# Performance work log

Hardware: AMD Instinct MI355X
Metric: run time of the kernel (lower is better)

## Reference

```python
import jax, jax.numpy as jnp
import numpy as np

WS = 8      # window size (all three entries equal)
NH = 4      # num_heads
CE = 32     # exp_channels = layer_size[0]


def _sine_pos(h, w, npf, temperature=10000.0):
    # faithful port of get_sine_position_encoding(HW=(h,w), num_pos_feats=npf, normalize=True)
    scale = 2.0 * np.pi
    eps = 1e-6
    y = np.cumsum(np.ones((1, h, w), np.float32), 1)
    xg = np.cumsum(np.ones((1, h, w), np.float32), 2)
    y = y / (y[:, -1:, :] + eps) * scale
    xg = xg / (xg[:, :, -1:] + eps) * scale
    dim_t = temperature ** (2.0 * (np.arange(npf) // 2) / npf)
    px = xg[..., None] / dim_t
    py = y[..., None] / dim_t
    px = np.stack((np.sin(px[..., 0::2]), np.cos(px[..., 1::2])), -1).reshape(1, h, w, npf)
    py = np.stack((np.sin(py[..., 0::2]), np.cos(py[..., 1::2])), -1).reshape(1, h, w, npf)
    return jnp.asarray(np.concatenate((py, px), -1).reshape(1, h * w, 2 * npf), jnp.float32)


def _rel_pos_index(a, b):
    coords = np.stack(np.meshgrid(np.arange(a), np.arange(b), indexing='ij')).reshape(2, -1)
    rel = (coords[:, :, None] - coords[:, None, :]).transpose(1, 2, 0).copy()
    rel[..., 0] += a - 1
    rel[..., 1] += b - 1
    rel[..., 0] *= 2 * b - 1
    return jnp.asarray(rel.sum(-1).astype(np.int32))


POS_BIAS = _sine_pos(WS, WS, CE // 2)   # (1, 64, 32)
RPI = _rel_pos_index(WS, WS)            # (64, 64) int


def _ln(x, g, b, eps=1e-5):
    mu = x.mean(-1, keepdims=True)
    var = jnp.mean((x - mu) ** 2, -1, keepdims=True)
    return (x - mu) / jnp.sqrt(var + eps) * g + b


def _geglu(x, w11, b11, w12, b12, w2, b2):
    return (jax.nn.gelu(x @ w11.T + b11, approximate=False) * (x @ w12.T + b12)) @ w2.T + b2


def _forward(x, ln1_g, ln1_b, w_ea, w_sa, rpb_table, fc11_w, fc11_b, fc12_w, fc12_b, fc2_w, fc2_b, ln2_g, ln2_b, m11_w, m11_b, m12_w, m12_b, m2_w, m2_b):
    B, E, C, H, W = x.shape
    h, w = H // WS, W // WS
    N = WS * WS
    nW = h * w
    scale = C ** (-0.5)
    x_origin = x
    # window partition (matches torch view/permute/contiguous-view exactly)
    xw = x.reshape(B, E, C, h, WS, w, WS).transpose(0, 1, 3, 5, 2, 4, 6).reshape(-1, N, C)
    xw = _ln(xw, ln1_g, ln1_b)
    # fused QKV projections
    qkv_ea = ((xw + POS_BIAS) @ w_ea.T).reshape(B, 4, nW, N, 3, NH, C)
    qkv_ea = qkv_ea.transpose(1, 4, 0, 2, 5, 3, 6).reshape(4, 3, B * nW, NH, N, C)   # E nP (B nW) nH W C
    qkv_sa = (xw @ w_sa.T).reshape(B, 4, nW, N, 3, NH, C)
    qkv_sa = qkv_sa.transpose(4, 0, 2, 5, 3, 1, 6).reshape(3, B * nW, NH, N, 4 * C)  # nP (B nW) nH W (E C)

    def attn(q, k, v, bias=None):
        s = jnp.einsum('bhid,bhjd->bhij', q * scale, k)
        if bias is not None:
            s = s + bias
        return jnp.einsum('bhij,bhjd->bhid', jax.nn.softmax(s, axis=-1), v)

    # exposure-alignment branches (the Python loop over 4 exposures, vectorized)
    ea1 = jax.vmap(attn, in_axes=(None, 0, 0))(qkv_ea[0, 0], qkv_ea[:, 1], qkv_ea[:, 2])
    ea2 = jax.vmap(attn, in_axes=(0, None, None))(qkv_ea[:, 0], qkv_ea[0, 1], qkv_ea[0, 2])

    def merge(o):  # (4, BnW, NH, N, C) -> cat over exposures on channels -> (BnW, N, NH*4C)
        o = jnp.moveaxis(o, 0, 3).reshape(B * nW, NH, N, 4 * C)
        return o.transpose(0, 2, 1, 3).reshape(B * nW, N, NH * 4 * C)

    ea1, ea2 = merge(ea1), merge(ea2)
    # self-attention branch with relative position bias gather
    bias = rpb_table[RPI.reshape(-1)].reshape(N, N, NH).transpose(2, 0, 1)[None]
    sa = attn(qkv_sa[0], qkv_sa[1], qkv_sa[2], bias)
    sa = sa.transpose(0, 2, 1, 3).reshape(B * nW, N, NH * 4 * C)

    y = jnp.concatenate([sa, ea1, ea2], axis=-1)                      # (BnW, N, 12*NH*C)
    y = _geglu(y, fc11_w, fc11_b, fc12_w, fc12_b, fc2_w, fc2_b)       # (BnW, N, 4C)
    # window reverse (matches torch view/permute/view exactly)
    y = y.reshape(B, h, w, WS, WS, 4, NH, C // NH).transpose(0, 5, 6, 7, 3, 1, 4, 2).reshape(B, 4, C, H, W)
    x1 = y + x_origin
    t = x1.transpose(0, 3, 4, 1, 2).reshape(B, H, W, 4 * C)           # B N C H W -> B H W (N C)
    t = _ln(t, ln2_g, ln2_b)
    t = _geglu(t, m11_w, m11_b, m12_w, m12_b, m2_w, m2_b)
    t = t.reshape(B, H, W, 4, C).transpose(0, 3, 4, 1, 2)
    return x1 + t


def setup_inputs() -> dict:
    key = jax.random.key(0)
    ks = jax.random.split(key, 10)
    f32 = jnp.float32
    return {
        'x': jax.random.normal(ks[0], (2, 4, 32, 128, 128), f32),
        'ln1_g': jnp.ones((32,), f32),
        'ln1_b': jnp.zeros((32,), f32),
        'w_ea': 0.02 * jax.random.normal(ks[1], (384, 32), f32),
        'w_sa': 0.02 * jax.random.normal(ks[2], (384, 32), f32),
        'rpb_table': 0.02 * jax.random.normal(ks[3], (225, 4), f32),
        'fc11_w': 0.02 * jax.random.normal(ks[4], (128, 1536), f32),
        'fc11_b': jnp.zeros((128,), f32),
        'fc12_w': 0.02 * jax.random.normal(ks[5], (128, 1536), f32),
        'fc12_b': jnp.zeros((128,), f32),
        'fc2_w': 0.02 * jax.random.normal(ks[6], (128, 128), f32),
        'fc2_b': jnp.zeros((128,), f32),
        'ln2_g': jnp.ones((128,), f32),
        'ln2_b': jnp.zeros((128,), f32),
        'm11_w': 0.02 * jax.random.normal(ks[7], (128, 128), f32),
        'm11_b': jnp.zeros((128,), f32),
        'm12_w': 0.02 * jax.random.normal(ks[8], (128, 128), f32),
        'm12_b': jnp.zeros((128,), f32),
        'm2_w': 0.02 * jax.random.normal(ks[9], (128, 128), f32),
        'm2_b': jnp.zeros((128,), f32),
    }


def reference(x, ln1_g, ln1_b, w_ea, w_sa, rpb_table, fc11_w, fc11_b, fc12_w, fc12_b, fc2_w, fc2_b, ln2_g, ln2_b, m11_w, m11_b, m12_w, m12_b, m2_w, m2_b):
    return _forward(x, ln1_g, ln1_b, w_ea, w_sa, rpb_table, fc11_w, fc11_b, fc12_w, fc12_b, fc2_w, fc2_b, ln2_g, ln2_b, m11_w, m11_b, m12_w, m12_b, m2_w, m2_b)
```

## Files before the change

### kernel.cpp

```cpp
#include <hip/hip_runtime.h>
#include <hip/hip_bf16.h>
#include <cstdint>

#define SCALE 0.17677669529663687f

typedef float f4v __attribute__((ext_vector_type(4)));
typedef short s4v __attribute__((ext_vector_type(4)));
typedef short short8 __attribute__((ext_vector_type(8)));

__device__ __forceinline__ float b2f(short s){
  return __uint_as_float(((unsigned)(unsigned short)s) << 16);
}
__device__ __forceinline__ short f2b(float f){
  __hip_bfloat16 h = __float2bfloat16(f);
  return *reinterpret_cast<short*>(&h);
}
__device__ __forceinline__ float geluf(float x){
  return 0.5f * x * (1.0f + erff(x * 0.7071067811865476f));
}
__device__ __forceinline__ f4v MFMA(short8 a, short8 b, f4v c){
  return __builtin_amdgcn_mfma_f32_16x16x32_bf16(a, b, c, 0, 0, 0);
}
__device__ __forceinline__ short8 ldsA(const short* base, int ld, int rowBase, int kBase, int l){
  return *(const short8*)(base + (rowBase + (l & 15)) * ld + kBase + ((l >> 4) << 3));
}
__device__ __forceinline__ short8 pack8(f4v a0, f4v a1, float scl){
  short8 o;
  #pragma unroll
  for (int k = 0; k < 4; ++k){
    o[k]     = f2b(a0[k] * scl);
    o[k + 4] = f2b(a1[k] * scl);
  }
  return o;
}
__device__ __forceinline__ int permTok(int n){
  return (n & 32) | (((n >> 2) & 3) << 3) | (((n >> 4) & 1) << 2) | (n & 3);
}

#define MTP_S   0
#define FWP1_S  8192
#define FWP2_S  204800
#define FC2_S   401408
#define M11_S   417792
#define M12_S   434176
#define M2_S    450560
#define POS_S   466944
#define BIASP_B 937984
#define AW_B    1048576

__global__ void prep(const float* __restrict__ wea, const float* __restrict__ wsa,
                     const float* __restrict__ fc11, const float* __restrict__ fc12,
                     const float* __restrict__ fc2,  const float* __restrict__ m11,
                     const float* __restrict__ m12,  const float* __restrict__ m2,
                     const float* __restrict__ rpb,
                     short* __restrict__ wsS, float* __restrict__ biasP)
{
  int gid = blockIdx.x * 256 + threadIdx.x;
  int stride = gridDim.x * 256;
  for (int id = gid; id < 786432; id += stride){
    int isB = (id >= 393216);
    int i2 = isB ? id - 393216 : id;
    const float* fc = isB ? fc12 : fc11;
    int blk = i2 >> 12, rem = i2 & 4095;
    int o = rem >> 5, s = rem & 31;
    int h4 = (s >> 3) & 3, kp = s & 7;
    int c = 16*(kp >> 2) + 4*h4 + (kp & 3);
    int br = blk >> 4, h = (blk >> 2) & 3, e = blk & 3;
    int cb = h*128 + e*32 + (br == 0 ? 0 : (br == 1 ? 512 : 1024));
    const float* w = (br == 0) ? wsa : wea;
    float acc = 0.f;
    for (int f = 0; f < 32; ++f)
      acc += fc[o*1536 + cb + f] * w[(256 + h*32 + f)*32 + c];
    wsS[(isB ? FWP2_S : FWP1_S) + blk*4096 + o*32 + s] = f2b(acc);
  }
  for (int id = gid; id < 8192; id += stride){
    int u = id >> 10, jp = (id >> 5) & 31, a = id & 31;
    int h = u & 3;
    const float* w = (u < 4) ? wsa : wea;
    int t = jp >> 4, h4 = (jp >> 2) & 3, r = jp & 3;
    int b = 8*h4 + 4*t + r;
    float acc = 0.f;
    for (int d = 0; d < 32; ++d)
      acc += w[(h*32 + d)*32 + a] * w[(128 + h*32 + d)*32 + b];
    wsS[MTP_S + u*1024 + jp*32 + a] = f2b(acc * SCALE);
  }
  for (int id = gid; id < 65536; id += stride){
    const float* src; int base; int off = id & 16383;
    switch (id >> 14){
      case 0:  src = fc2; base = FC2_S; break;
      case 1:  src = m11; base = M11_S; break;
      case 2:  src = m12; base = M12_S; break;
      default: src = m2;  base = M2_S;  break;
    }
    wsS[base + off] = f2b(src[off]);
  }
  for (int id = gid; id < 16384; id += stride){
    int hh = id >> 12, i = (id >> 6) & 63, h4 = (id >> 4) & 3, tj = (id >> 2) & 3, r = id & 3;
    int j = tj*16 + 4*h4 + r;
    int idx = ((i >> 3) - (j >> 3) + 7)*15 + ((i & 7) - (j & 7) + 7);
    biasP[id] = rpb[idx*4 + hh];
  }
  if (gid < 64){
    const float invT[8] = {1.f, 0.316227766f, 0.1f, 0.0316227766f,
                           0.01f, 0.00316227766f, 0.001f, 0.000316227766f};
    const float ANG = 6.28318530717958647692f / 8.000001f;
    float ay = (float)((gid >> 3) + 1) * ANG;
    float ax = (float)((gid & 7) + 1) * ANG;
    #pragma unroll
    for (int m = 0; m < 8; ++m){
      float s, cc;
      sincosf(ay * invT[m], &s, &cc);
      wsS[POS_S + gid*32 + 2*m]      = f2b(s);
      wsS[POS_S + gid*32 + 2*m + 1]  = f2b(cc);
      sincosf(ax * invT[m], &s, &cc);
      wsS[POS_S + gid*32 + 16 + 2*m] = f2b(s);
      wsS[POS_S + gid*32 + 17 + 2*m] = f2b(cc);
    }
  }
}

struct __align__(16) SmemA {
  short xw[8192];
  short xtp[9216];
};

__device__ __forceinline__ float smax16(f4v &s0, f4v &s1, f4v &s2, f4v &s3){
  float m = s0[0];
  #pragma unroll
  for (int r = 0; r < 4; ++r){
    m = fmaxf(m, s0[r]); m = fmaxf(m, s1[r]);
    m = fmaxf(m, s2[r]); m = fmaxf(m, s3[r]);
  }
  m = fmaxf(m, __shfl_xor(m, 16));
  m = fmaxf(m, __shfl_xor(m, 32));
  float sum = 0.f;
  #pragma unroll
  for (int r = 0; r < 4; ++r){
    float e0 = __expf(s0[r] - m), e1 = __expf(s1[r] - m);
    float e2 = __expf(s2[r] - m), e3 = __expf(s3[r] - m);
    s0[r] = e0; s1[r] = e1; s2[r] = e2; s3[r] = e3;
    sum += e0 + e1 + e2 + e3;
  }
  sum += __shfl_xor(sum, 16);
  sum += __shfl_xor(sum, 32);
  return __builtin_amdgcn_rcpf(sum);
}

__device__ __forceinline__ short8 projXq(const short* mtp, const short* xwE,
                                         int rho, int l){
  short8 xa = *(const short8*)(xwE + (rho*16 + (l & 15))*32 + ((l >> 4) << 3));
  f4v q0 = {0.f,0.f,0.f,0.f}, q1 = {0.f,0.f,0.f,0.f};
  q0 = MFMA(*(const short8*)(mtp + (l & 15)*32 + ((l >> 4) << 3)), xa, q0);
  q1 = MFMA(*(const short8*)(mtp + (16 + (l & 15))*32 + ((l >> 4) << 3)), xa, q1);
  return pack8(q0, q1, 1.f);
}

__device__ __forceinline__ void geglu8(short8 rp, const short* wsS, int blk, int beta,
                                       f4v &g10, f4v &g11, f4v &g12, f4v &g13,
                                       f4v &g20, f4v &g21, f4v &g22, f4v &g23, int l){
  const short* f1 = wsS + FWP1_S + blk*4096 + beta*2048 + (l & 15)*32 + ((l >> 4) << 3);
  g10 = MFMA(rp, *(const short8*)(f1 +    0), g10);
  g11 = MFMA(rp, *(const short8*)(f1 +  512), g11);
  g12 = MFMA(rp, *(const short8*)(f1 + 1024), g12);
  g13 = MFMA(rp, *(const short8*)(f1 + 1536), g13);
  const short* f2 = wsS + FWP2_S + blk*4096 + beta*2048 + (l & 15)*32 + ((l >> 4) << 3);
  g20 = MFMA(rp, *(const short8*)(f2 +    0), g20);
  g21 = MFMA(rp, *(const short8*)(f2 +  512), g21);
  g22 = MFMA(rp, *(const short8*)(f2 + 1024), g22);
  g23 = MFMA(rp, *(const short8*)(f2 + 1536), g23);
}

__device__ __forceinline__ void unitTail(f4v s0, f4v s1, f4v s2, f4v s3,
                                         const short* xtpE, const short* wsS,
                                         int blk, int blkFold, int beta,
                                         f4v &g10, f4v &g11, f4v &g12, f4v &g13,
                                         f4v &g20, f4v &g21, f4v &g22, f4v &g23, int l){
  float inv = smax16(s0, s1, s2, s3);
  short8 pk0 = pack8(s0, s1, 1.f);
  short8 pk1 = pack8(s2, s3, 1.f);
  f4v rt0 = {0.f,0.f,0.f,0.f}, rt1 = {0.f,0.f,0.f,0.f};
  const short* x0 = xtpE + (l & 15)*72 + ((l >> 4) << 3);
  const short* x1 = xtpE + (16 + (l & 15))*72 + ((l >> 4) << 3);
  rt0 = MFMA(*(const short8*)(x0), pk0, rt0);
  rt0 = MFMA(*(const short8*)(x0 + 32), pk1, rt0);
  rt1 = MFMA(*(const short8*)(x1), pk0, rt1);
  rt1 = MFMA(*(const short8*)(x1 + 32), pk1, rt1);
  short8 rp = pack8(rt0, rt1, inv);
  geglu8(rp, wsS, blk, beta, g10, g11, g12, g13, g20, g21, g22, g23, l);
  if (blkFold >= 0)
    geglu8(rp, wsS, blkFold, beta, g10, g11, g12, g13, g20, g21, g22, g23, l);
}

__global__ __launch_bounds__(256, 3) void kernelA(
    const float* __restrict__ x,
    const float* __restrict__ ln1g, const float* __restrict__ ln1b,
    const float* __restrict__ fc11b_, const float* __restrict__ fc12b_,
    const short* __restrict__ wsS, const float* __restrict__ biasP,
    short* __restrict__ aw)
{
  __shared__ SmemA sm;
  short* xw  = sm.xw;
  short* xtp = sm.xtp;

  const int t = threadIdx.x, l = t & 63, w = t >> 6;
  const int rho = w;
  const int bw = ((blockIdx.x & 7) << 7) | (blockIdx.x >> 3);
  const int win = bw >> 1, beta = bw & 1;
  const int b = win >> 8, hw = win & 255, hi = hw >> 4, wj = hw & 15;
  const int row0 = rho*16 + ((l >> 4) << 2);
  const short* posb = wsS + POS_S;

  {
    const int e = w, n = l;
    const int c = n >> 1, i0 = (n & 1) * 4;
    const float* src = x + ((size_t)((b*4 + e)*32 + c) * 128 + hi*8) * 128 + wj*8;
    float sum = 0.f, ssq = 0.f;
    #pragma unroll
    for (int ii = 0; ii < 4; ++ii){
      f4v a  = *(const f4v*)(src + (size_t)(i0 + ii)*128);
      f4v bb = *(const f4v*)(src + (size_t)(i0 + ii)*128 + 4);
      #pragma unroll
      for (int k = 0; k < 4; ++k){
        sum += a[k] + bb[k];
        ssq += a[k]*a[k] + bb[k]*bb[k];
      }
    }
    float mu = sum * (1.f/32.f);
    float rstd = rsqrtf(ssq * (1.f/32.f) - mu*mu + 1e-5f);
    int pn = permTok(n);
    #pragma unroll
    for (int ii = 0; ii < 4; ++ii){
      f4v a  = *(const f4v*)(src + (size_t)(i0 + ii)*128);
      f4v bb = *(const f4v*)(src + (size_t)(i0 + ii)*128 + 4);
      s4v o0, o1;
      #pragma unroll
      for (int k = 0; k < 4; ++k){
        int ch = ii*8 + k;
        o0[k] = f2b((a[k]  - mu)*rstd*ln1g[ch]     + ln1b[ch]);
        o1[k] = f2b((bb[k] - mu)*rstd*ln1g[ch + 4] + ln1b[ch + 4]);
      }
      *(s4v*)&xw[e*2048 + n*32 + ii*8]     = o0;
      *(s4v*)&xw[e*2048 + n*32 + ii*8 + 4] = o1;
      #pragma unroll
      for (int k = 0; k < 4; ++k){
        xtp[e*2304 + (ii*8 + k)*72 + pn]     = o0[k];
        xtp[e*2304 + (ii*8 + k + 4)*72 + pn] = o1[k];
      }
    }
  }
  __syncthreads();

  f4v g10 = {0.f,0.f,0.f,0.f}, g11 = {0.f,0.f,0.f,0.f};
  f4v g12 = {0.f,0.f,0.f,0.f}, g13 = {0.f,0.f,0.f,0.f};
  f4v g20 = {0.f,0.f,0.f,0.f}, g21 = {0.f,0.f,0.f,0.f};
  f4v g22 = {0.f,0.f,0.f,0.f}, g23 = {0.f,0.f,0.f,0.f};

  #pragma unroll 1
  for (int hh = 0; hh < 4; ++hh){
    const short* mtp = wsS + MTP_S + hh*1024;
    f4v s0 = {0.f,0.f,0.f,0.f}, s1 = {0.f,0.f,0.f,0.f};
    f4v s2 = {0.f,0.f,0.f,0.f}, s3 = {0.f,0.f,0.f,0.f};
    #pragma unroll
    for (int e = 0; e < 4; ++e){
      short8 xq = projXq(mtp, xw + e*2048, rho, l);
      s0 = MFMA(ldsA(xw + e*2048, 32,  0, 0, l), xq, s0);
      s1 = MFMA(ldsA(xw + e*2048, 32, 16, 0, l), xq, s1);
      s2 = MFMA(ldsA(xw + e*2048, 32, 32, 0, l), xq, s2);
      s3 = MFMA(ldsA(xw + e*2048, 32, 48, 0, l), xq, s3);
    }
    const float* bb = biasP + ((hh*64 + rho*16 + (l & 15))*4 + (l >> 4)) * 16;
    s0 += *(const f4v*)(bb);
    s1 += *(const f4v*)(bb + 4);
    s2 += *(const f4v*)(bb + 8);
    s3 += *(const f4v*)(bb + 12);
    float inv = smax16(s0, s1, s2, s3);
    short8 pk0 = pack8(s0, s1, 1.f);
    short8 pk1 = pack8(s2, s3, 1.f);
    #pragma unroll 1
    for (int dc = 0; dc < 4; ++dc){
      const short* xt = xtp + dc*2304;
      f4v rt0 = {0.f,0.f,0.f,0.f}, rt1 = {0.f,0.f,0.f,0.f};
      const short* x0 = xt + (l & 15)*72 + ((l >> 4) << 3);
      const short* x1 = xt + (16 + (l & 15))*72 + ((l >> 4) << 3);
      rt0 = MFMA(*(const short8*)(x0), pk0, rt0);
      rt0 = MFMA(*(const short8*)(x0 + 32), pk1, rt0);
      rt1 = MFMA(*(const short8*)(x1), pk0, rt1);
      rt1 = MFMA(*(const short8*)(x1 + 32), pk1, rt1);
      short8 rp = pack8(rt0, rt1, inv);
      geglu8(rp, wsS, hh*4 + dc, beta,
             g10, g11, g12, g13, g20, g21, g22, g23, l);
    }
  }

  __syncthreads();
  {
    const int e = w, n = l;
    #pragma unroll
    for (int c4 = 0; c4 < 8; ++c4){
      s4v xa = *(const s4v*)&xw[e*2048 + n*32 + c4*4];
      s4v pa = *(const s4v*)(posb + n*32 + c4*4);
      s4v o;
      #pragma unroll
      for (int j = 0; j < 4; ++j) o[j] = f2b(b2f(xa[j]) + b2f(pa[j]));
      *(s4v*)&xw[e*2048 + n*32 + c4*4] = o;
    }
    int pn = permTok(n);
    #pragma unroll
    for (int c2 = 0; c2 < 32; ++c2){
      int idx = e*2304 + c2*72 + pn;
      xtp[idx] = f2b(b2f(xtp[idx]) + b2f(posb[n*32 + c2]));
    }
  }
  __syncthreads();

  #pragma unroll 1
  for (int hh = 0; hh < 4; ++hh){
    const short* mtp = wsS + MTP_S + (4 + hh)*1024;
    #pragma unroll 1
    for (int e = 0; e < 4; ++e){
      short8 xq = projXq(mtp, xw + e*2048, rho, l);
      f4v s0 = {0.f,0.f,0.f,0.f}, s1 = {0.f,0.f,0.f,0.f};
      f4v s2 = {0.f,0.f,0.f,0.f}, s3 = {0.f,0.f,0.f,0.f};
      s0 = MFMA(ldsA(xw, 32,  0, 0, l), xq, s0);
      s1 = MFMA(ldsA(xw, 32, 16, 0, l), xq, s1);
      s2 = MFMA(ldsA(xw, 32, 32, 0, l), xq, s2);
      s3 = MFMA(ldsA(xw, 32, 48, 0, l), xq, s3);
      unitTail(s0, s1, s2, s3, xtp, wsS,
               32 + hh*4 + e, (e == 0) ? (16 + hh*4) : -1, beta,
               g10, g11, g12, g13, g20, g21, g22, g23, l);
    }
    short8 xq0 = projXq(mtp, xw, rho, l);
    #pragma unroll 1
    for (int e = 1; e < 4; ++e){
      f4v s0 = {0.f,0.f,0.f,0.f}, s1 = {0.f,0.f,0.f,0.f};
      f4v s2 = {0.f,0.f,0.f,0.f}, s3 = {0.f,0.f,0.f,0.f};
      s0 = MFMA(ldsA(xw + e*2048, 32,  0, 0, l), xq0, s0);
      s1 = MFMA(ldsA(xw + e*2048, 32, 16, 0, l), xq0, s1);
      s2 = MFMA(ldsA(xw + e*2048, 32, 32, 0, l), xq0, s2);
      s3 = MFMA(ldsA(xw + e*2048, 32, 48, 0, l), xq0, s3);
      unitTail(s0, s1, s2, s3, xtp + e*2304, wsS,
               16 + hh*4 + e, -1, beta,
               g10, g11, g12, g13, g20, g21, g22, g23, l);
    }
  }

  {
    short* awb = aw + (size_t)win * 8192 + beta*64;
    auto epi = [&](int ct, f4v G1, f4v G2){
      int ol = ct*16 + (l & 15);
      int og = beta*64 + ol;
      float b1 = fc11b_[og], b2 = fc12b_[og];
      #pragma unroll
      for (int r = 0; r < 4; ++r)
        awb[(row0 + r)*128 + ol] = f2b(geluf(G1[r] + b1) * (G2[r] + b2));
    };
    epi(0, g10, g20);
    epi(1, g11, g21);
    epi(2, g12, g22);
    epi(3, g13, g23);
  }
}

struct __align__(16) SmemB {
  float x1t[128][66];
  short apx[64][136];
  short xnt[64][136];
};

__global__ __launch_bounds__(256, 2) void kernelB(
    const float* __restrict__ x,
    const float* __restrict__ fc2b_,
    const float* __restrict__ ln2g, const float* __restrict__ ln2b,
    const float* __restrict__ m11b, const float* __restrict__ m12b,
    const float* __restrict__ m2b,
    const short* __restrict__ wsS, const short* __restrict__ aw,
    float* __restrict__ out)
{
  __shared__ SmemB sm;
  const int t = threadIdx.x, l = t & 63, w = t >> 6;
  const int id = blockIdx.x;
  const int b = id >> 8, rr = (id >> 1) & 127, chi = id & 1;
  const short* fc2 = wsS + FC2_S;
  const short* m11 = wsS + M11_S;
  const short* m12 = wsS + M12_S;
  const short* m2  = wsS + M2_S;

  {
    const float* xb = x + (size_t)b * 2097152 + (size_t)rr * 128 + chi*64;
    for (int fid = t; fid < 2048; fid += 256){
      int ch = fid >> 4, q4 = fid & 15;
      *(f4v*)&sm.x1t[ch][q4*4] = *(const f4v*)(xb + (size_t)ch * 16384 + q4*4);
    }
  }
  {
    int pl = t >> 2, oq = t & 3;
    int pxg = chi*64 + pl;
    int winl = b*256 + (rr & 15)*16 + (pxg & 15);
    int tok  = (rr >> 4)*8 + (pxg >> 4);
    const short* as = aw + (size_t)winl * 8192 + tok*128 + oq*32;
    #pragma unroll
    for (int k8 = 0; k8 < 4; ++k8)
      *(short8*)&sm.apx[pl][oq*32 + k8*8] = *(const short8*)(as + k8*8);
  }
  __syncthreads();
  {
    f4v z[8];
    #pragma unroll
    for (int i = 0; i < 8; ++i) z[i] = (f4v){0.f,0.f,0.f,0.f};
    #pragma unroll
    for (int ks = 0; ks < 4; ++ks){
      short8 a = ldsA(&sm.apx[0][0], 136, w*16, ks*32, l);
      const short* pB = fc2 + (l & 15)*128 + ks*32 + ((l >> 4) << 3);
      #pragma unroll
      for (int ct = 0; ct < 8; ++ct)
        z[ct] = MFMA(a, *(const short8*)(pB + ct*16*128), z[ct]);
    }
    #pragma unroll
    for (int ct = 0; ct < 8; ++ct){
      int ch = ct*16 + (l & 15);
      float bz = fc2b_[ch];
      #pragma unroll
      for (int r = 0; r < 4; ++r){
        int px = w*16 + ((l >> 4) << 2) + r;
        sm.x1t[ch][px] += z[ct][r] + bz;
      }
    }
  }
  __syncthreads();
  {
    int pl = t >> 2, qd = t & 3;
    float s = 0.f;
    for (int i = 0; i < 32; ++i) s += sm.x1t[qd*32 + i][pl];
    s += __shfl_xor(s, 1);
    s += __shfl_xor(s, 2);
    float mu = s * (1.f/128.f);
    float vv = 0.f;
    for (int i = 0; i < 32; ++i){ float d = sm.x1t[qd*32 + i][pl] - mu; vv += d*d; }
    vv += __shfl_xor(vv, 1);
    vv += __shfl_xor(vv, 2);
    float rstd = rsqrtf(vv * (1.f/128.f) + 1e-5f);
    for (int i4 = 0; i4 < 8; ++i4){
      s4v o;
      #pragma unroll
      for (int j = 0; j < 4; ++j){
        int ch = qd*32 + i4*4 + j;
        o[j] = f2b((sm.x1t[ch][pl] - mu) * rstd * ln2g[ch] + ln2b[ch]);
      }
      *(s4v*)&sm.xnt[pl][qd*32 + i4*4] = o;
    }
  }
  __syncthreads();
  {
    f4v G1[8], G2[8];
    #pragma unroll
    for (int i = 0; i < 8; ++i){
      G1[i] = (f4v){0.f,0.f,0.f,0.f};
      G2[i] = (f4v){0.f,0.f,0.f,0.f};
    }
    #pragma unroll
    for (int ks = 0; ks < 4; ++ks){
      short8 a = ldsA(&sm.xnt[0][0], 136, w*16, ks*32, l);
      const short* p1 = m11 + (l & 15)*128 + ks*32 + ((l >> 4) << 3);
      #pragma unroll
      for (int ct = 0; ct < 8; ++ct)
        G1[ct] = MFMA(a, *(const short8*)(p1 + ct*16*128), G1[ct]);
      const short* p2 = m12 + (l & 15)*128 + ks*32 + ((l >> 4) << 3);
      #pragma unroll
      for (int ct = 0; ct < 8; ++ct)
        G2[ct] = MFMA(a, *(const short8*)(p2 + ct*16*128), G2[ct]);
    }
    int r0 = w*16 + ((l >> 4) << 2);
    #pragma unroll
    for (int ct = 0; ct < 8; ++ct){
      int o = ct*16 + (l & 15);
      float bb1 = m11b[o], bb2 = m12b[o];
      #pragma unroll
      for (int r = 0; r < 4; ++r)
        sm.apx[r0 + r][o] = f2b(geluf(G1[ct][r] + bb1) * (G2[ct][r] + bb2));
    }
  }
  __syncthreads();
  {
    f4v Z[8];
    #pragma unroll
    for (int i = 0; i < 8; ++i) Z[i] = (f4v){0.f,0.f,0.f,0.f};
    #pragma unroll
    for (int ks = 0; ks < 4; ++ks){
      short8 a = ldsA(&sm.apx[0][0], 136, w*16, ks*32, l);
      const short* pz = m2 + (l & 15)*128 + ks*32 + ((l >> 4) << 3);
      #pragma unroll
      for (int ct = 0; ct < 8; ++ct)
        Z[ct] = MFMA(a, *(const short8*)(pz + ct*16*128), Z[ct]);
    }
    #pragma unroll
    for (int ct = 0; ct < 8; ++ct){
      int ch = ct*16 + (l & 15);
      float bz = m2b[ch];
      #pragma unroll
      for (int r = 0; r < 4; ++r){
        int px = w*16 + ((l >> 4) << 2) + r;
        sm.x1t[ch][px] += Z[ct][r] + bz;
      }
    }
  }
  __syncthreads();
  {
    int ch = t >> 1, qh = t & 1;
    float* ob = out + ((size_t)b*128 + ch) * 16384 + (size_t)rr * 128 + chi*64 + qh*32;
    #pragma unroll
    for (int q4 = 0; q4 < 8; ++q4)
      *(f4v*)(ob + q4*4) = *(const f4v*)&sm.x1t[ch][qh*32 + q4*4];
  }
}

extern "C" void kernel_launch(void* const* d_in, const int* in_sizes, int n_in,
                              void* d_out, int out_size, void* d_ws, size_t ws_size,
                              hipStream_t stream) {
  (void)in_sizes; (void)n_in; (void)out_size; (void)ws_size;
  const float* x     = (const float*)d_in[0];
  const float* ln1g  = (const float*)d_in[1];
  const float* ln1b  = (const float*)d_in[2];
  const float* wea   = (const float*)d_in[3];
  const float* wsa   = (const float*)d_in[4];
  const float* rpb   = (const float*)d_in[5];
  const float* fc11w = (const float*)d_in[6];
  const float* fc11b = (const float*)d_in[7];
  const float* fc12w = (const float*)d_in[8];
  const float* fc12b = (const float*)d_in[9];
  const float* fc2w  = (const float*)d_in[10];
  const float* fc2b  = (const float*)d_in[11];
  const float* ln2g  = (const float*)d_in[12];
  const float* ln2b  = (const float*)d_in[13];
  const float* m11w  = (const float*)d_in[14];
  const float* m11b  = (const float*)d_in[15];
  const float* m12w  = (const float*)d_in[16];
  const float* m12b  = (const float*)d_in[17];
  const float* m2w   = (const float*)d_in[18];
  const float* m2b   = (const float*)d_in[19];

  short* wsS   = (short*)d_ws;
  float* biasP = (float*)((char*)d_ws + BIASP_B);
  short* aw    = (short*)((char*)d_ws + AW_B);

  prep<<<1024, 256, 0, stream>>>(wea, wsa, fc11w, fc12w, fc2w, m11w, m12w, m2w,
                                 rpb, wsS, biasP);
  kernelA<<<1024, 256, 0, stream>>>(x, ln1g, ln1b, fc11b, fc12b,
                                    wsS, biasP, aw);
  kernelB<<<512, 256, 0, stream>>>(x, fc2b, ln2g, ln2b, m11b, m12b, m2b,
                                   wsS, aw, (float*)d_out);
}
```

Baseline: 202.6 us.

## Batch attention heads per pass to reuse LDS fragments and expose MFMA ILP

The first attention phase now computes the score tiles for all four heads together. Each key fragment loaded from LDS is reused across the four heads, and each xtp fragment is reused across heads in the PV/GEGLU loop. The second phase hoists the key and query fragments out of the head loop and computes the four score sets per head in one batch before the softmax and tail. This cuts LDS reads and gives the scheduler more independent MFMAs, but it raises register pressure, so launch bounds drop from 3 to 2 blocks per CU, which may lower occupancy.

New measurement: 204.8 us. Within noise of the previous version (+1.1%).

```diff
diff --git a/kernel.cpp b/kernel.cpp
--- a/kernel.cpp
+++ b/kernel.cpp
@@ -146,9 +146,7 @@
   return __builtin_amdgcn_rcpf(sum);
 }
 
-__device__ __forceinline__ short8 projXq(const short* mtp, const short* xwE,
-                                         int rho, int l){
-  short8 xa = *(const short8*)(xwE + (rho*16 + (l & 15))*32 + ((l >> 4) << 3));
+__device__ __forceinline__ short8 projXqF(const short* mtp, short8 xa, int l){
   f4v q0 = {0.f,0.f,0.f,0.f}, q1 = {0.f,0.f,0.f,0.f};
   q0 = MFMA(*(const short8*)(mtp + (l & 15)*32 + ((l >> 4) << 3)), xa, q0);
   q1 = MFMA(*(const short8*)(mtp + (16 + (l & 15))*32 + ((l >> 4) << 3)), xa, q1);
@@ -170,28 +168,7 @@
   g23 = MFMA(rp, *(const short8*)(f2 + 1536), g23);
 }
 
-__device__ __forceinline__ void unitTail(f4v s0, f4v s1, f4v s2, f4v s3,
-                                         const short* xtpE, const short* wsS,
-                                         int blk, int blkFold, int beta,
-                                         f4v &g10, f4v &g11, f4v &g12, f4v &g13,
-                                         f4v &g20, f4v &g21, f4v &g22, f4v &g23, int l){
-  float inv = smax16(s0, s1, s2, s3);
-  short8 pk0 = pack8(s0, s1, 1.f);
-  short8 pk1 = pack8(s2, s3, 1.f);
-  f4v rt0 = {0.f,0.f,0.f,0.f}, rt1 = {0.f,0.f,0.f,0.f};
-  const short* x0 = xtpE + (l & 15)*72 + ((l >> 4) << 3);
-  const short* x1 = xtpE + (16 + (l & 15))*72 + ((l >> 4) << 3);
-  rt0 = MFMA(*(const short8*)(x0), pk0, rt0);
-  rt0 = MFMA(*(const short8*)(x0 + 32), pk1, rt0);
-  rt1 = MFMA(*(const short8*)(x1), pk0, rt1);
-  rt1 = MFMA(*(const short8*)(x1 + 32), pk1, rt1);
-  short8 rp = pack8(rt0, rt1, inv);
-  geglu8(rp, wsS, blk, beta, g10, g11, g12, g13, g20, g21, g22, g23, l);
-  if (blkFold >= 0)
-    geglu8(rp, wsS, blkFold, beta, g10, g11, g12, g13, g20, g21, g22, g23, l);
-}
-
-__global__ __launch_bounds__(256, 3) void kernelA(
+__global__ __launch_bounds__(256, 2) void kernelA(
     const float* __restrict__ x,
     const float* __restrict__ ln1g, const float* __restrict__ ln1b,
     const float* __restrict__ fc11b_, const float* __restrict__ fc12b_,
@@ -206,23 +183,23 @@
   const int rho = w;
   const int bw = ((blockIdx.x & 7) << 7) | (blockIdx.x >> 3);
   const int win = bw >> 1, beta = bw & 1;
-  const int b = win >> 8, hw = win & 255, hi = hw >> 4, wj = hw & 15;
+  const int bb_ = win >> 8, hw = win & 255, hi = hw >> 4, wj = hw & 15;
   const int row0 = rho*16 + ((l >> 4) << 2);
   const short* posb = wsS + POS_S;
 
   {
     const int e = w, n = l;
     const int c = n >> 1, i0 = (n & 1) * 4;
-    const float* src = x + ((size_t)((b*4 + e)*32 + c) * 128 + hi*8) * 128 + wj*8;
+    const float* src = x + ((size_t)((bb_*4 + e)*32 + c) * 128 + hi*8) * 128 + wj*8;
     float sum = 0.f, ssq = 0.f;
     #pragma unroll
     for (int ii = 0; ii < 4; ++ii){
       f4v a  = *(const f4v*)(src + (size_t)(i0 + ii)*128);
-      f4v bb = *(const f4v*)(src + (size_t)(i0 + ii)*128 + 4);
+      f4v bbv = *(const f4v*)(src + (size_t)(i0 + ii)*128 + 4);
       #pragma unroll
       for (int k = 0; k < 4; ++k){
-        sum += a[k] + bb[k];
-        ssq += a[k]*a[k] + bb[k]*bb[k];
+        sum += a[k] + bbv[k];
+        ssq += a[k]*a[k] + bbv[k]*bbv[k];
       }
     }
     float mu = sum * (1.f/32.f);
@@ -231,13 +208,13 @@
     #pragma unroll
     for (int ii = 0; ii < 4; ++ii){
       f4v a  = *(const f4v*)(src + (size_t)(i0 + ii)*128);
-      f4v bb = *(const f4v*)(src + (size_t)(i0 + ii)*128 + 4);
+      f4v bbv = *(const f4v*)(src + (size_t)(i0 + ii)*128 + 4);
       s4v o0, o1;
       #pragma unroll
       for (int k = 0; k < 4; ++k){
         int ch = ii*8 + k;
-        o0[k] = f2b((a[k]  - mu)*rstd*ln1g[ch]     + ln1b[ch]);
-        o1[k] = f2b((bb[k] - mu)*rstd*ln1g[ch + 4] + ln1b[ch + 4]);
+        o0[k] = f2b((a[k]   - mu)*rstd*ln1g[ch]     + ln1b[ch]);
+        o1[k] = f2b((bbv[k] - mu)*rstd*ln1g[ch + 4] + ln1b[ch + 4]);
       }
       *(s4v*)&xw[e*2048 + n*32 + ii*8]     = o0;
       *(s4v*)&xw[e*2048 + n*32 + ii*8 + 4] = o1;
@@ -255,40 +232,62 @@
   f4v g20 = {0.f,0.f,0.f,0.f}, g21 = {0.f,0.f,0.f,0.f};
   f4v g22 = {0.f,0.f,0.f,0.f}, g23 = {0.f,0.f,0.f,0.f};
 
-  #pragma unroll 1
-  for (int hh = 0; hh < 4; ++hh){
-    const short* mtp = wsS + MTP_S + hh*1024;
-    f4v s0 = {0.f,0.f,0.f,0.f}, s1 = {0.f,0.f,0.f,0.f};
-    f4v s2 = {0.f,0.f,0.f,0.f}, s3 = {0.f,0.f,0.f,0.f};
+  {
+    f4v s[4][4];
+    #pragma unroll
+    for (int h = 0; h < 4; ++h)
+      #pragma unroll
+      for (int tj = 0; tj < 4; ++tj) s[h][tj] = (f4v){0.f,0.f,0.f,0.f};
     #pragma unroll
     for (int e = 0; e < 4; ++e){
-      short8 xq = projXq(mtp, xw + e*2048, rho, l);
-      s0 = MFMA(ldsA(xw + e*2048, 32,  0, 0, l), xq, s0);
-      s1 = MFMA(ldsA(xw + e*2048, 32, 16, 0, l), xq, s1);
-      s2 = MFMA(ldsA(xw + e*2048, 32, 32, 0, l), xq, s2);
-      s3 = MFMA(ldsA(xw + e*2048, 32, 48, 0, l), xq, s3);
-    }
-    const float* bb = biasP + ((hh*64 + rho*16 + (l & 15))*4 + (l >> 4)) * 16;
-    s0 += *(const f4v*)(bb);
-    s1 += *(const f4v*)(bb + 4);
-    s2 += *(const f4v*)(bb + 8);
-    s3 += *(const f4v*)(bb + 12);
-    float inv = smax16(s0, s1, s2, s3);
-    short8 pk0 = pack8(s0, s1, 1.f);
-    short8 pk1 = pack8(s2, s3, 1.f);
+      const short* xwE = xw + e*2048;
+      short8 xa = *(const short8*)(xwE + (rho*16 + (l & 15))*32 + ((l >> 4) << 3));
+      short8 xq0 = projXqF(wsS + MTP_S,        xa, l);
+      short8 xq1 = projXqF(wsS + MTP_S + 1024, xa, l);
+      short8 xq2 = projXqF(wsS + MTP_S + 2048, xa, l);
+      short8 xq3 = projXqF(wsS + MTP_S + 3072, xa, l);
+      #pragma unroll
+      for (int tj = 0; tj < 4; ++tj){
+        short8 kf = ldsA(xwE, 32, tj*16, 0, l);
+        s[0][tj] = MFMA(kf, xq0, s[0][tj]);
+        s[1][tj] = MFMA(kf, xq1, s[1][tj]);
+        s[2][tj] = MFMA(kf, xq2, s[2][tj]);
+        s[3][tj] = MFMA(kf, xq3, s[3][tj]);
+      }
+    }
+    float inv[4];
+    short8 pk[4][2];
+    #pragma unroll
+    for (int h = 0; h < 4; ++h){
+      const float* bp = biasP + ((h*64 + rho*16 + (l & 15))*4 + (l >> 4)) * 16;
+      s[h][0] += *(const f4v*)(bp);
+      s[h][1] += *(const f4v*)(bp + 4);
+      s[h][2] += *(const f4v*)(bp + 8);
+      s[h][3] += *(const f4v*)(bp + 12);
+      inv[h] = smax16(s[h][0], s[h][1], s[h][2], s[h][3]);
+      pk[h][0] = pack8(s[h][0], s[h][1], 1.f);
+      pk[h][1] = pack8(s[h][2], s[h][3], 1.f);
+    }
     #pragma unroll 1
     for (int dc = 0; dc < 4; ++dc){
       const short* xt = xtp + dc*2304;
-      f4v rt0 = {0.f,0.f,0.f,0.f}, rt1 = {0.f,0.f,0.f,0.f};
-      const short* x0 = xt + (l & 15)*72 + ((l >> 4) << 3);
-      const short* x1 = xt + (16 + (l & 15))*72 + ((l >> 4) << 3);
-      rt0 = MFMA(*(const short8*)(x0), pk0, rt0);
-      rt0 = MFMA(*(const short8*)(x0 + 32), pk1, rt0);
-      rt1 = MFMA(*(const short8*)(x1), pk0, rt1);
-      rt1 = MFMA(*(const short8*)(x1 + 32), pk1, rt1);
-      short8 rp = pack8(rt0, rt1, inv);
-      geglu8(rp, wsS, hh*4 + dc, beta,
-             g10, g11, g12, g13, g20, g21, g22, g23, l);
+      const short* x0p = xt + (l & 15)*72 + ((l >> 4) << 3);
+      const short* x1p = xt + (16 + (l & 15))*72 + ((l >> 4) << 3);
+      short8 f00 = *(const short8*)(x0p);
+      short8 f01 = *(const short8*)(x0p + 32);
+      short8 f10 = *(const short8*)(x1p);
+      short8 f11 = *(const short8*)(x1p + 32);
+      #pragma unroll
+      for (int h = 0; h < 4; ++h){
+        f4v rt0 = {0.f,0.f,0.f,0.f}, rt1 = {0.f,0.f,0.f,0.f};
+        rt0 = MFMA(f00, pk[h][0], rt0);
+        rt0 = MFMA(f01, pk[h][1], rt0);
+        rt1 = MFMA(f10, pk[h][0], rt1);
+        rt1 = MFMA(f11, pk[h][1], rt1);
+        short8 rp = pack8(rt0, rt1, inv[h]);
+        geglu8(rp, wsS, h*4 + dc, beta,
+               g10, g11, g12, g13, g20, g21, g22, g23, l);
+      }
     }
   }
 
@@ -313,34 +312,104 @@
   }
   __syncthreads();
 
-  #pragma unroll 1
-  for (int hh = 0; hh < 4; ++hh){
-    const short* mtp = wsS + MTP_S + (4 + hh)*1024;
+  {
+    short8 ke0 = ldsA(xw, 32,  0, 0, l);
+    short8 ke1 = ldsA(xw, 32, 16, 0, l);
+    short8 ke2 = ldsA(xw, 32, 32, 0, l);
+    short8 ke3 = ldsA(xw, 32, 48, 0, l);
+    short8 xa0 = *(const short8*)(xw +        (rho*16 + (l & 15))*32 + ((l >> 4) << 3));
+    short8 xa1 = *(const short8*)(xw + 2048 + (rho*16 + (l & 15))*32 + ((l >> 4) << 3));
+    short8 xa2 = *(const short8*)(xw + 4096 + (rho*16 + (l & 15))*32 + ((l >> 4) << 3));
+    short8 xa3 = *(const short8*)(xw + 6144 + (rho*16 + (l & 15))*32 + ((l >> 4) << 3));
+
     #pragma unroll 1
-    for (int e = 0; e < 4; ++e){
-      short8 xq = projXq(mtp, xw + e*2048, rho, l);
-      f4v s0 = {0.f,0.f,0.f,0.f}, s1 = {0.f,0.f,0.f,0.f};
-      f4v s2 = {0.f,0.f,0.f,0.f}, s3 = {0.f,0.f,0.f,0.f};
-      s0 = MFMA(ldsA(xw, 32,  0, 0, l), xq, s0);
-      s1 = MFMA(ldsA(xw, 32, 16, 0, l), xq, s1);
-      s2 = MFMA(ldsA(xw, 32, 32, 0, l), xq, s2);
-      s3 = MFMA(ldsA(xw, 32, 48, 0, l), xq, s3);
-      unitTail(s0, s1, s2, s3, xtp, wsS,
-               32 + hh*4 + e, (e == 0) ? (16 + hh*4) : -1, beta,
-               g10, g11, g12, g13, g20, g21, g22, g23, l);
-    }
-    short8 xq0 = projXq(mtp, xw, rho, l);
-    #pragma unroll 1
-    for (int e = 1; e < 4; ++e){
-      f4v s0 = {0.f,0.f,0.f,0.f}, s1 = {0.f,0.f,0.f,0.f};
-      f4v s2 = {0.f,0.f,0.f,0.f}, s3 = {0.f,0.f,0.f,0.f};
-      s0 = MFMA(ldsA(xw + e*2048, 32,  0, 0, l), xq0, s0);
-      s1 = MFMA(ldsA(xw + e*2048, 32, 16, 0, l), xq0, s1);
-      s2 = MFMA(ldsA(xw + e*2048, 32, 32, 0, l), xq0, s2);
-      s3 = MFMA(ldsA(xw + e*2048, 32, 48, 0, l), xq0, s3);
-      unitTail(s0, s1, s2, s3, xtp + e*2304, wsS,
-               16 + hh*4 + e, -1, beta,
-               g10, g11, g12, g13, g20, g21, g22, g23, l);
+    for (int hh = 0; hh < 4; ++hh){
+      const short* mtp = wsS + MTP_S + (4 + hh)*1024;
+      short8 xq0 = projXqF(mtp, xa0, l);
+      short8 xq1 = projXqF(mtp, xa1, l);
+      short8 xq2 = projXqF(mtp, xa2, l);
+      short8 xq3 = projXqF(mtp, xa3, l);
+      {
+        f4v s[4][4];
+        #pragma unroll
+        for (int e = 0; e < 4; ++e)
+          #pragma unroll
+          for (int tj = 0; tj < 4; ++tj) s[e][tj] = (f4v){0.f,0.f,0.f,0.f};
+        s[0][0]=MFMA(ke0,xq0,s[0][0]); s[1][0]=MFMA(ke0,xq1,s[1][0]);
+        s[2][0]=MFMA(ke0,xq2,s[2][0]); s[3][0]=MFMA(ke0,xq3,s[3][0]);
+        s[0][1]=MFMA(ke1,xq0,s[0][1]); s[1][1]=MFMA(ke1,xq1,s[1][1]);
+        s[2][1]=MFMA(ke1,xq2,s[2][1]); s[3][1]=MFMA(ke1,xq3,s[3][1]);
+        s[0][2]=MFMA(ke2,xq0,s[0][2]); s[1][2]=MFMA(ke2,xq1,s[1][2]);
+        s[2][2]=MFMA(ke2,xq2,s[2][2]); s[3][2]=MFMA(ke2,xq3,s[3][2]);
+        s[0][3]=MFMA(ke3,xq0,s[0][3]); s[1][3]=MFMA(ke3,xq1,s[1][3]);
+        s[2][3]=MFMA(ke3,xq2,s[2][3]); s[3][3]=MFMA(ke3,xq3,s[3][3]);
+        float inv[4];
+        short8 pk[4][2];
+        #pragma unroll
+        for (int e = 0; e < 4; ++e){
+          inv[e] = smax16(s[e][0], s[e][1], s[e][2], s[e][3]);
+          pk[e][0] = pack8(s[e][0], s[e][1], 1.f);
+          pk[e][1] = pack8(s[e][2], s[e][3], 1.f);
+        }
+        const short* x0p = xtp + (l & 15)*72 + ((l >> 4) << 3);
+        const short* x1p = xtp + (16 + (l & 15))*72 + ((l >> 4) << 3);
+        short8 f00 = *(const short8*)(x0p);
+        short8 f01 = *(const short8*)(x0p + 32);
+        short8 f10 = *(const short8*)(x1p);
+        short8 f11 = *(const short8*)(x1p + 32);
+        #pragma unroll
+        for (int e = 0; e < 4; ++e){
+          f4v rt0 = {0.f,0.f,0.f,0.f}, rt1 = {0.f,0.f,0.f,0.f};
+          rt0 = MFMA(f00, pk[e][0], rt0);
+          rt0 = MFMA(f01, pk[e][1], rt0);
+          rt1 = MFMA(f10, pk[e][0], rt1);
+          rt1 = MFMA(f11, pk[e][1], rt1);
+          short8 rp = pack8(rt0, rt1, inv[e]);
+          geglu8(rp, wsS, 32 + hh*4 + e, beta,
+                 g10, g11, g12, g13, g20, g21, g22, g23, l);
+          if (e == 0)
+            geglu8(rp, wsS, 16 + hh*4, beta,
+                   g10, g11, g12, g13, g20, g21, g22, g23, l);
+        }
+      }
+      {
+        f4v s[3][4];
+        #pragma unroll
+        for (int ei = 0; ei < 3; ++ei)
+          #pragma unroll
+          for (int tj = 0; tj < 4; ++tj) s[ei][tj] = (f4v){0.f,0.f,0.f,0.f};
+        #pragma unroll
+        for (int ei = 0; ei < 3; ++ei){
+          const short* xwE = xw + (ei + 1)*2048;
+          #pragma unroll
+          for (int tj = 0; tj < 4; ++tj){
+            short8 kf = ldsA(xwE, 32, tj*16, 0, l);
+            s[ei][tj] = MFMA(kf, xq0, s[ei][tj]);
+          }
+        }
+        float inv[3];
+        short8 pk[3][2];
+        #pragma unroll
+        for (int ei = 0; ei < 3; ++ei){
+          inv[ei] = smax16(s[ei][0], s[ei][1], s[ei][2], s[ei][3]);
+          pk[ei][0] = pack8(s[ei][0], s[ei][1], 1.f);
+          pk[ei][1] = pack8(s[ei][2], s[ei][3], 1.f);
+        }
+        #pragma unroll
+        for (int ei = 0; ei < 3; ++ei){
+          const short* xt = xtp + (ei + 1)*2304;
+          const short* x0p = xt + (l & 15)*72 + ((l >> 4) << 3);
+          const short* x1p = xt + (16 + (l & 15))*72 + ((l >> 4) << 3);
+          f4v rt0 = {0.f,0.f,0.f,0.f}, rt1 = {0.f,0.f,0.f,0.f};
+          rt0 = MFMA(*(const short8*)(x0p), pk[ei][0], rt0);
+          rt0 = MFMA(*(const short8*)(x0p + 32), pk[ei][1], rt0);
+          rt1 = MFMA(*(const short8*)(x1p), pk[ei][0], rt1);
+          rt1 = MFMA(*(const short8*)(x1p + 32), pk[ei][1], rt1);
+          short8 rp = pack8(rt0, rt1, inv[ei]);
+          geglu8(rp, wsS, 16 + hh*4 + ei + 1, beta,
+                 g10, g11, g12, g13, g20, g21, g22, g23, l);
+        }
+      }
     }
   }
 
```
